# Performance work log

Hardware: AMD Instinct MI355X
Metric: run time of the kernel (lower is better)

## Reference

```python
import jax, jax.numpy as jnp
import numpy as np

B, NQ, NC, D, H = 4, 4096, 4096, 1024, 16
HD = D // H
LN_EPS = 1e-5


def _layernorm(x, g, b):
    mu = jnp.mean(x, axis=-1, keepdims=True)
    var = jnp.var(x, axis=-1, keepdims=True)
    return (x - mu) * jax.lax.rsqrt(var + LN_EPS) * g + b


def _kernel(x):
    # elu(x) + 1  (strictly positive feature map)
    return jax.nn.elu(x) + 1.0


def setup_inputs() -> dict:
    key = jax.random.key(0)
    ks = jax.random.split(key, 12)
    s = 1.0 / np.sqrt(D)
    return {
        "query": jax.random.normal(ks[0], (B, NQ, D), jnp.float32),
        "context": jax.random.normal(ks[1], (B, NC, D), jnp.float32),
        "q_w": jax.random.uniform(ks[2], (D, D), jnp.float32, -s, s),
        "q_b": jnp.zeros((D,), jnp.float32),
        "k_w": jax.random.uniform(ks[3], (D, D), jnp.float32, -s, s),
        "k_b": jnp.zeros((D,), jnp.float32),
        "v_w": jax.random.uniform(ks[4], (D, D), jnp.float32, -s, s),
        "v_b": jnp.zeros((D,), jnp.float32),
        "o_w": jax.random.uniform(ks[5], (D, D), jnp.float32, -s, s),
        "o_b": jnp.zeros((D,), jnp.float32),
        "lnq_g": jnp.ones((D,), jnp.float32),
        "lnq_b": jnp.zeros((D,), jnp.float32),
        "lnkv_g": jnp.ones((D,), jnp.float32),
        "lnkv_b": jnp.zeros((D,), jnp.float32),
    }


def reference(query, context, q_w, q_b, k_w, k_b, v_w, v_b, o_w, o_b,
              lnq_g, lnq_b, lnkv_g, lnkv_b):
    residual = query
    q = _layernorm(query, lnq_g, lnq_b)
    c = _layernorm(context, lnkv_g, lnkv_b)

    # torch Linear: y = x @ W.T + b ; reshape to (B, H, N, Hd)
    Q = (q @ q_w.T + q_b).reshape(B, NQ, H, HD).transpose(0, 2, 1, 3)
    K = (c @ k_w.T + k_b).reshape(B, NC, H, HD).transpose(0, 2, 1, 3)
    V = (c @ v_w.T + v_b).reshape(B, NC, H, HD).transpose(0, 2, 1, 3)

    Q = _kernel(Q)
    K = _kernel(K)

    # KV: (B, H, Hd, Hd) outer-product accumulation over context length
    KV = jnp.einsum("bhnd,bhne->bhde", K, V)
    K_sum = K.sum(axis=2)                              # (B, H, Hd)
    Z = jnp.einsum("bhqd,bhd->bhq", Q, K_sum)          # (B, H, Nq)
    Z = jnp.maximum(Z, 1e-6)

    out = jnp.einsum("bhqd,bhde->bhqe", Q, KV) / Z[..., None]
    out = out.transpose(0, 2, 1, 3).reshape(B, NQ, D)
    return residual + (out @ o_w.T + o_b)
```

## Files before the change

### kernel.cpp

```cpp
#include <hip/hip_runtime.h>

#define DEV __device__ __forceinline__

typedef __attribute__((ext_vector_type(8))) short short8;
typedef __attribute__((ext_vector_type(4))) short short4v;
typedef __attribute__((ext_vector_type(4))) float f32x4;

DEV float bf2f(unsigned short u) { return __uint_as_float(((unsigned int)u) << 16); }
DEV unsigned short f2bf(float f) {
    unsigned int u = __float_as_uint(f);
    u += 0x7FFFu + ((u >> 16) & 1u);
    return (unsigned short)(u >> 16);
}

DEV float elu1(float v) { return v > 0.0f ? v + 1.0f : __expf(v); }

DEV void gload_lds16(const void* g, void* l) {
    __builtin_amdgcn_global_load_lds(
        (__attribute__((address_space(1))) unsigned int*)(g),
        (__attribute__((address_space(3))) unsigned int*)(l),
        16, 0, 0);
}

#define NROW 16384
#define DDIM 1024

__global__ __launch_bounds__(256) void ln_kernel(
    const float* __restrict__ query, const float* __restrict__ context,
    const float* __restrict__ lnq_g, const float* __restrict__ lnq_b,
    const float* __restrict__ lnk_g, const float* __restrict__ lnk_b,
    unsigned short* __restrict__ qln, unsigned short* __restrict__ cln,
    const float* __restrict__ q_w, const float* __restrict__ k_w,
    const float* __restrict__ v_w, const float* __restrict__ o_w,
    unsigned short* __restrict__ wout)
{
    const int tid = threadIdx.x;
    if (blockIdx.x >= 2 * NROW) {
        const int i = (blockIdx.x - 2 * NROW) * 256 + tid;
        const int mat = i >> 18;
        const int idx = (i & 262143) * 4;
        const float* src = mat == 0 ? q_w : mat == 1 ? k_w : mat == 2 ? v_w : o_w;
        f32x4 v = *(const f32x4*)(src + idx);
        short4v o;
#pragma unroll
        for (int j = 0; j < 4; ++j) o[j] = (short)f2bf(v[j]);
        *(short4v*)(wout + (size_t)mat * 1048576 + idx) = o;
        return;
    }

    const int row = blockIdx.x;
    const bool isq = row < NROW;
    const int r = isq ? row : row - NROW;
    const float* src = (isq ? query : context) + (size_t)r * DDIM;
    const float* g   = isq ? lnq_g : lnk_g;
    const float* bb  = isq ? lnq_b : lnk_b;
    unsigned short* dst = (isq ? qln : cln) + (size_t)r * DDIM;

    f32x4 x = *(const f32x4*)(src + tid * 4);
    float s  = x[0] + x[1] + x[2] + x[3];
    float sq = x[0]*x[0] + x[1]*x[1] + x[2]*x[2] + x[3]*x[3];
#pragma unroll
    for (int off = 32; off; off >>= 1) {
        s  += __shfl_xor(s, off);
        sq += __shfl_xor(sq, off);
    }
    __shared__ float red[8];
    const int lane = tid & 63, w = tid >> 6;
    if (lane == 0) { red[w] = s; red[4 + w] = sq; }
    __syncthreads();
    s  = red[0] + red[1] + red[2] + red[3];
    sq = red[4] + red[5] + red[6] + red[7];
    const float mu  = s * (1.0f / DDIM);
    const float var = sq * (1.0f / DDIM) - mu * mu;
    const float rstd = rsqrtf(var + 1e-5f);

    f32x4 gv = *(const f32x4*)(g + tid * 4);
    f32x4 bv = *(const f32x4*)(bb + tid * 4);
    short4v o;
#pragma unroll
    for (int j = 0; j < 4; ++j)
        o[j] = (short)f2bf((x[j] - mu) * rstd * gv[j] + bv[j]);
    *(short4v*)(dst + tid * 4) = o;
}

template <typename EPI>
DEV void gemm128(unsigned short* __restrict__ sA,
                 unsigned short* __restrict__ sB,
                 const unsigned short* __restrict__ Ap,
                 const unsigned short* __restrict__ Bp,
                 int m0, int n0, EPI epi)
{
    const int tid = threadIdx.x;
    const int lane = tid & 63, w = tid >> 6;
    const int wr = w >> 1, wc = w & 1;
    const int lr = lane & 15, lg = lane >> 4;

    const int srow = tid >> 3;
    const int cswz = (tid & 7) ^ (srow & 7);
    const unsigned short* gA0 = Ap + (size_t)(m0 + srow) * 1024 + cswz * 8;
    const unsigned short* gB0 = Bp + (size_t)(n0 + srow) * 1024 + cswz * 8;
    unsigned short* dA = sA + tid * 8;
    unsigned short* dB = sB + tid * 8;

    const int sw0 = ((0 + lg) ^ (lr & 7)) * 8;
    const int sw1 = ((4 + lg) ^ (lr & 7)) * 8;

    f32x4 acc[4][4];
#pragma unroll
    for (int i = 0; i < 4; ++i)
#pragma unroll
        for (int j = 0; j < 4; ++j)
#pragma unroll
            for (int e = 0; e < 4; ++e) acc[i][j][e] = 0.0f;

#define STG8(T)                                                               \
    {                                                                         \
        const int ko = (T) * 64;                                              \
        _Pragma("unroll")                                                     \
        for (int j = 0; j < 4; ++j) {                                         \
            gload_lds16(gA0 + ko + (size_t)j * 32768, dA + j * 2048);         \
            gload_lds16(gB0 + ko + (size_t)j * 32768, dB + j * 2048);         \
        }                                                                     \
    }

    STG8(0);
    for (int t = 0; t < 16; ++t) {
        asm volatile("s_waitcnt vmcnt(0)" ::: "memory");
        __builtin_amdgcn_s_barrier();

        short8 af[4], bf[4];
#pragma unroll
        for (int mt = 0; mt < 4; ++mt)
            af[mt] = *(const short8*)&sA[(wr * 64 + mt * 16 + lr) * 64 + sw0];
#pragma unroll
        for (int nt = 0; nt < 4; ++nt)
            bf[nt] = *(const short8*)&sB[(wc * 64 + nt * 16 + lr) * 64 + sw0];
        __builtin_amdgcn_s_setprio(1);
#pragma unroll
        for (int mt = 0; mt < 4; ++mt)
#pragma unroll
            for (int nt = 0; nt < 4; ++nt)
                acc[mt][nt] = __builtin_amdgcn_mfma_f32_16x16x32_bf16(
                    af[mt], bf[nt], acc[mt][nt], 0, 0, 0);
        __builtin_amdgcn_s_setprio(0);

#pragma unroll
        for (int mt = 0; mt < 4; ++mt)
            af[mt] = *(const short8*)&sA[(wr * 64 + mt * 16 + lr) * 64 + sw1];
#pragma unroll
        for (int nt = 0; nt < 4; ++nt)
            bf[nt] = *(const short8*)&sB[(wc * 64 + nt * 16 + lr) * 64 + sw1];
        asm volatile("s_waitcnt lgkmcnt(0)" ::: "memory");
        __builtin_amdgcn_s_barrier();
        if (t < 15) STG8(t + 1);
        __builtin_amdgcn_s_setprio(1);
#pragma unroll
        for (int mt = 0; mt < 4; ++mt)
#pragma unroll
            for (int nt = 0; nt < 4; ++nt)
                acc[mt][nt] = __builtin_amdgcn_mfma_f32_16x16x32_bf16(
                    af[mt], bf[nt], acc[mt][nt], 0, 0, 0);
        __builtin_amdgcn_s_setprio(0);
    }
#undef STG8

#pragma unroll
    for (int mt = 0; mt < 4; ++mt)
#pragma unroll
        for (int nt = 0; nt < 4; ++nt) {
            const int col = n0 + wc * 64 + nt * 16 + lr;
#pragma unroll
            for (int i = 0; i < 4; ++i) {
                const int row = m0 + wr * 64 + mt * 16 + lg * 4 + i;
                epi(row, col, acc[mt][nt][i]);
            }
        }
}

__global__ __launch_bounds__(256, 4) void gemm_qkv(
    const unsigned short* __restrict__ QLN, const unsigned short* __restrict__ WQ,
    const unsigned short* __restrict__ CLN, const unsigned short* __restrict__ WKV,
    unsigned short* __restrict__ Qm, unsigned short* __restrict__ KVT,
    const float* __restrict__ q_b, const float* __restrict__ k_b,
    const float* __restrict__ v_b)
{
    __shared__ __attribute__((aligned(16))) unsigned short sA[128 * 64];
    __shared__ __attribute__((aligned(16))) unsigned short sB[128 * 64];

    const int bid = blockIdx.x;
    const int l = (bid & 7) * 384 + (bid >> 3);

    if (l < 1024) {
        const int m0 = (l >> 3) * 128, n0 = (l & 7) * 128;
        gemm128(sA, sB, QLN, WQ, m0, n0,
            [&](int row, int col, float v) {
                v = elu1(v + q_b[col]);
                Qm[(size_t)row * 1024 + col] = f2bf(v);
            });
    } else {
        const int r = l - 1024;
        const int m0 = (r & 15) * 128, n0 = (r >> 4) * 128;
        gemm128(sA, sB, WKV, CLN, m0, n0,
            [&](int row, int col, float v) {
                if (row < 1024) v = elu1(v + k_b[row]);
                else            v = v + v_b[row - 1024];
                KVT[(size_t)row * NROW + col] = f2bf(v);
            });
    }
}

__global__ __launch_bounds__(512, 2) void gemm_out256(
    const unsigned short* __restrict__ A, const unsigned short* __restrict__ Bm,
    float* __restrict__ Cout, const float* __restrict__ bias,
    const float* __restrict__ resid)
{
    __shared__ __attribute__((aligned(16))) unsigned short smem[65536];
    unsigned short* sAb = smem;
    unsigned short* sBb = smem + 32768;

    const int bid = blockIdx.x;
    const int l = (bid & 7) * 32 + (bid >> 3);
    const int m0 = (l >> 2) * 256, n0 = (l & 3) * 256;

    const int tid = threadIdx.x;
    const int lane = tid & 63, w = tid >> 6;
    const int wr = w >> 2, wc = w & 3;
    const int lr = lane & 15, lg = lane >> 4;

    const int srow = tid >> 3;
    const int cswz = (tid & 7) ^ (srow & 7);
    const unsigned short* gA0 = A  + (size_t)(m0 + srow) * 1024 + cswz * 8;
    const unsigned short* gB0 = Bm + (size_t)(n0 + srow) * 1024 + cswz * 8;

    const int sw0 = ((0 + lg) ^ (lr & 7)) * 8;
    const int sw1 = ((4 + lg) ^ (lr & 7)) * 8;

    f32x4 acc[8][4];
#pragma unroll
    for (int i = 0; i < 8; ++i)
#pragma unroll
        for (int j = 0; j < 4; ++j)
#pragma unroll
            for (int e = 0; e < 4; ++e) acc[i][j][e] = 0.0f;

#define STG(GP, SP, T)                                                        \
    {                                                                         \
        const unsigned short* g = (GP) + (T) * 64;                            \
        unsigned short* d = (SP) + ((T) & 1) * 16384 + tid * 8;               \
        _Pragma("unroll")                                                     \
        for (int L = 0; L < 4; ++L)                                           \
            gload_lds16(g + (size_t)L * 65536, d + L * 4096);                 \
    }

    STG(gB0, sBb, 0); STG(gA0, sAb, 0); STG(gB0, sBb, 1); STG(gA0, sAb, 1);
    asm volatile("s_waitcnt vmcnt(8)" ::: "memory");
    __builtin_amdgcn_s_barrier();

    short8 bvl[2][2];
#pragma unroll
    for (int nt = 0; nt < 2; ++nt) {
        const int rb = (wc * 64 + nt * 16 + lr) * 64;
        bvl[nt][0] = *(const short8*)&sBb[rb + sw0];
        bvl[nt][1] = *(const short8*)&sBb[rb + sw1];
    }

    for (int t = 0; t < 16; ++t) {
        const unsigned short* bA = sAb + (t & 1) * 16384;
        const unsigned short* bB = sBb + (t & 1) * 16384;
        const unsigned short* bBn = sBb + ((t + 1) & 1) * 16384;
        short8 afl[4][2], afh[4][2], bvh[2][2], bvln[2][2];

#pragma unroll
        for (int mt = 0; mt < 4; ++mt) {
            const int ra = (wr * 128 + mt * 16 + lr) * 64;
            afl[mt][0] = *(const short8*)&bA[ra + sw0];
            afl[mt][1] = *(const short8*)&bA[ra + sw1];
        }
#pragma unroll
        for (int mt = 0; mt < 4; ++mt) {
            const int ra = (wr * 128 + (mt + 4) * 16 + lr) * 64;
            afh[mt][0] = *(const short8*)&bA[ra + sw0];
            afh[mt][1] = *(const short8*)&bA[ra + sw1];
        }
        asm volatile("s_waitcnt lgkmcnt(8)" ::: "memory");
        __builtin_amdgcn_s_setprio(1);
#pragma unroll
        for (int kk = 0; kk < 2; ++kk)
#pragma unroll
            for (int mt = 0; mt < 4; ++mt)
#pragma unroll
                for (int nt = 0; nt < 2; ++nt)
                    acc[mt][nt] = __builtin_amdgcn_mfma_f32_16x16x32_bf16(
                        afl[mt][kk], bvl[nt][kk], acc[mt][nt], 0, 0, 0);
        __builtin_amdgcn_s_setprio(0);
        __builtin_amdgcn_s_barrier();

#pragma unroll
        for (int nt = 0; nt < 2; ++nt) {
            const int rb = (wc * 64 + (nt + 2) * 16 + lr) * 64;
            bvh[nt][0] = *(const short8*)&bB[rb + sw0];
            bvh[nt][1] = *(const short8*)&bB[rb + sw1];
        }
        asm volatile("s_waitcnt lgkmcnt(4)" ::: "memory");
        __builtin_amdgcn_s_setprio(1);
#pragma unroll
        for (int kk = 0; kk < 2; ++kk)
#pragma unroll
            for (int mt = 0; mt < 4; ++mt)
#pragma unroll
                for (int nt = 0; nt < 2; ++nt)
                    acc[mt + 4][nt] = __builtin_amdgcn_mfma_f32_16x16x32_bf16(
                        afh[mt][kk], bvl[nt][kk], acc[mt + 4][nt], 0, 0, 0);
        __builtin_amdgcn_s_setprio(0);
        asm volatile("s_waitcnt vmcnt(0)" ::: "memory");
        __builtin_amdgcn_s_barrier();

        if (t < 15) {
#pragma unroll
            for (int nt = 0; nt < 2; ++nt) {
                const int rb = (wc * 64 + nt * 16 + lr) * 64;
                bvln[nt][0] = *(const short8*)&bBn[rb + sw0];
                bvln[nt][1] = *(const short8*)&bBn[rb + sw1];
            }
        }
        if (t + 2 < 16) STG(gA0, sAb, t + 2);
        if (t < 15) asm volatile("s_waitcnt lgkmcnt(4)" ::: "memory");
        else        asm volatile("s_waitcnt lgkmcnt(0)" ::: "memory");
        __builtin_amdgcn_s_setprio(1);
#pragma unroll
        for (int kk = 0; kk < 2; ++kk)
#pragma unroll
            for (int mt = 0; mt < 4; ++mt)
#pragma unroll
                for (int nt = 0; nt < 2; ++nt)
                    acc[mt + 4][nt + 2] = __builtin_amdgcn_mfma_f32_16x16x32_bf16(
                        afh[mt][kk], bvh[nt][kk], acc[mt + 4][nt + 2], 0, 0, 0);
        __builtin_amdgcn_s_setprio(0);
        __builtin_amdgcn_s_barrier();

        if (t + 2 < 16) STG(gB0, sBb, t + 2);
        __builtin_amdgcn_s_setprio(1);
#pragma unroll
        for (int kk = 0; kk < 2; ++kk)
#pragma unroll
            for (int mt = 0; mt < 4; ++mt)
#pragma unroll
                for (int nt = 0; nt < 2; ++nt)
                    acc[mt][nt + 2] = __builtin_amdgcn_mfma_f32_16x16x32_bf16(
                        afl[mt][kk], bvh[nt][kk], acc[mt][nt + 2], 0, 0, 0);
        __builtin_amdgcn_s_setprio(0);

        if (t < 15) {
#pragma unroll
            for (int nt = 0; nt < 2; ++nt) {
                bvl[nt][0] = bvln[nt][0];
                bvl[nt][1] = bvln[nt][1];
            }
        }
    }
#undef STG

#pragma unroll
    for (int mt = 0; mt < 8; ++mt) {
#pragma unroll
        for (int nt = 0; nt < 4; ++nt) {
            const int col = n0 + wc * 64 + nt * 16 + lr;
#pragma unroll
            for (int i = 0; i < 4; ++i) {
                const int row = m0 + wr * 128 + mt * 16 + lg * 4 + i;
                Cout[(size_t)row * 1024 + col] =
                    acc[mt][nt][i] + bias[col] + resid[(size_t)row * 1024 + col];
            }
        }
    }
}

__global__ __launch_bounds__(256) void kv_kernel(
    const unsigned short* __restrict__ VT, const unsigned short* __restrict__ KT,
    float* __restrict__ KVTp, float* __restrict__ Ksump)
{
    const int bh = blockIdx.x, sp = blockIdx.y;
    const int b = bh >> 4, h = bh & 15;
    const int tid = threadIdx.x, lane = tid & 63, w = tid >> 6;
    const int lr = lane & 15, lg = lane >> 4;

    f32x4 acc[4][4];
#pragma unroll
    for (int i = 0; i < 4; ++i)
#pragma unroll
        for (int j = 0; j < 4; ++j)
#pragma unroll
            for (int e = 0; e < 4; ++e) acc[i][j][e] = 0.0f;
    float kp[4] = {0.0f, 0.0f, 0.0f, 0.0f};

    const size_t colbase = (size_t)b * 4096 + sp * 512 + w * 128 + lg * 8;
    const unsigned short* va = VT + (size_t)(h * 64 + lr) * NROW + colbase;
    const unsigned short* ka = KT + (size_t)(h * 64 + lr) * NROW + colbase;

    for (int ks = 0; ks < 4; ++ks) {
        short8 af[4], bfv[4];
#pragma unroll
        for (int mt = 0; mt < 4; ++mt)
            af[mt] = *(const short8*)(va + (size_t)mt * 16 * NROW + ks * 32);
#pragma unroll
        for (int nt = 0; nt < 4; ++nt)
            bfv[nt] = *(const short8*)(ka + (size_t)nt * 16 * NROW + ks * 32);
#pragma unroll
        for (int mt = 0; mt < 4; ++mt)
#pragma unroll
            for (int nt = 0; nt < 4; ++nt)
                acc[mt][nt] = __builtin_amdgcn_mfma_f32_16x16x32_bf16(
                    af[mt], bfv[nt], acc[mt][nt], 0, 0, 0);
#pragma unroll
        for (int nt = 0; nt < 4; ++nt)
#pragma unroll
            for (int j = 0; j < 8; ++j)
                kp[nt] += bf2f((unsigned short)bfv[nt][j]);
    }

#pragma unroll
    for (int nt = 0; nt < 4; ++nt) {
        kp[nt] += __shfl_xor(kp[nt], 16);
        kp[nt] += __shfl_xor(kp[nt], 32);
    }
    __shared__ float kred[4][64];
    if (lane < 16) {
#pragma unroll
        for (int nt = 0; nt < 4; ++nt) kred[w][nt * 16 + lane] = kp[nt];
    }

    __shared__ float red4[4][4096];
#pragma unroll
    for (int mt = 0; mt < 4; ++mt)
#pragma unroll
        for (int nt = 0; nt < 4; ++nt)
#pragma unroll
            for (int i = 0; i < 4; ++i)
                red4[w][(mt * 16 + lg * 4 + i) * 64 + nt * 16 + lr] = acc[mt][nt][i];
    __syncthreads();
    float* out = KVTp + ((size_t)sp * 64 + bh) * 4096;
    for (int i = tid; i < 4096; i += 256)
        out[i] = red4[0][i] + red4[1][i] + red4[2][i] + red4[3][i];
    if (tid < 64)
        Ksump[((size_t)sp * 64 + bh) * 64 + tid] =
            kred[0][tid] + kred[1][tid] + kred[2][tid] + kred[3][tid];
}

__global__ __launch_bounds__(256) void kvred_kernel(
    const float* __restrict__ KVTp, const float* __restrict__ Ksump,
    float* __restrict__ KVs, float* __restrict__ Ks)
{
    const int bh = blockIdx.x;
    const int tid = threadIdx.x;
    for (int i = tid * 4; i < 4096; i += 1024) {
        f32x4 s = {0.0f, 0.0f, 0.0f, 0.0f};
#pragma unroll
        for (int sp = 0; sp < 8; ++sp) {
            f32x4 v = *(const f32x4*)(KVTp + ((size_t)sp * 64 + bh) * 4096 + i);
            s[0] += v[0]; s[1] += v[1]; s[2] += v[2]; s[3] += v[3];
        }
        *(f32x4*)(KVs + (size_t)bh * 4096 + i) = s;
    }
    if (tid < 64) {
        float s = 0.0f;
#pragma unroll
        for (int sp = 0; sp < 8; ++sp)
            s += Ksump[((size_t)sp * 64 + bh) * 64 + tid];
        Ks[bh * 64 + tid] = s;
    }
}

__global__ __launch_bounds__(256) void a2_kernel(
    const unsigned short* __restrict__ Q, const float* __restrict__ KVs,
    const float* __restrict__ Ks, unsigned short* __restrict__ A2)
{
    const int m0 = blockIdx.x * 128, h = blockIdx.y;
    const int b = m0 >> 12, bh = (b << 4) + h;
    const int tid = threadIdx.x, lane = tid & 63, w = tid >> 6;
    const int wr = w >> 1, wc = w & 1;
    const int lr = lane & 15, lg = lane >> 4;

    __shared__ float ksum_s[64];
    if (tid < 64) ksum_s[tid] = Ks[bh * 64 + tid];
    __syncthreads();

    f32x4 acc[4][2];
#pragma unroll
    for (int i = 0; i < 4; ++i)
#pragma unroll
        for (int j = 0; j < 2; ++j)
#pragma unroll
            for (int e = 0; e < 4; ++e) acc[i][j][e] = 0.0f;
    float zp[4] = {0.0f, 0.0f, 0.0f, 0.0f};

    const unsigned short* qa = Q + (size_t)(m0 + wr * 64 + lr) * DDIM + h * 64 + lg * 8;
    const float* kvb = KVs + (size_t)bh * 4096 + (wc * 32 + lr) * 64 + lg * 8;

#pragma unroll
    for (int ks = 0; ks < 2; ++ks) {
        short8 af[4];
#pragma unroll
        for (int mt = 0; mt < 4; ++mt)
            af[mt] = *(const short8*)(qa + (size_t)mt * 16 * DDIM + ks * 32);
#pragma unroll
        for (int mt = 0; mt < 4; ++mt)
#pragma unroll
            for (int j = 0; j < 8; ++j)
                zp[mt] += bf2f((unsigned short)af[mt][j]) * ksum_s[ks * 32 + lg * 8 + j];
        short8 bfv[2];
#pragma unroll
        for (int nt = 0; nt < 2; ++nt) {
            const float* p = kvb + nt * 16 * 64 + ks * 32;
            f32x4 v0 = *(const f32x4*)(p);
            f32x4 v1 = *(const f32x4*)(p + 4);
            short8 t;
#pragma unroll
            for (int j = 0; j < 4; ++j) {
                t[j]     = (short)f2bf(v0[j]);
                t[j + 4] = (short)f2bf(v1[j]);
            }
            bfv[nt] = t;
        }
#pragma unroll
        for (int mt = 0; mt < 4; ++mt)
#pragma unroll
            for (int nt = 0; nt < 2; ++nt)
                acc[mt][nt] = __builtin_amdgcn_mfma_f32_16x16x32_bf16(
                    af[mt], bfv[nt], acc[mt][nt], 0, 0, 0);
    }

    float zinv[4];
#pragma unroll
    for (int mt = 0; mt < 4; ++mt) {
        zp[mt] += __shfl_xor(zp[mt], 16);
        zp[mt] += __shfl_xor(zp[mt], 32);
        zinv[mt] = 1.0f / fmaxf(zp[mt], 1e-6f);
    }

#pragma unroll
    for (int mt = 0; mt < 4; ++mt)
#pragma unroll
        for (int nt = 0; nt < 2; ++nt)
#pragma unroll
            for (int i = 0; i < 4; ++i) {
                const int row = m0 + wr * 64 + mt * 16 + lg * 4 + i;
                const int col = h * 64 + wc * 32 + nt * 16 + lr;
                const float zi = __shfl(zinv[mt], lg * 4 + i);
                const float v = acc[mt][nt][i] * zi;
                A2[(size_t)row * DDIM + col] = f2bf(v);
            }
}

extern "C" void kernel_launch(void* const* d_in, const int* in_sizes, int n_in,
                              void* d_out, int out_size, void* d_ws, size_t ws_size,
                              hipStream_t stream)
{
    const float* query   = (const float*)d_in[0];
    const float* context = (const float*)d_in[1];
    const float* q_w = (const float*)d_in[2];
    const float* q_b = (const float*)d_in[3];
    const float* k_w = (const float*)d_in[4];
    const float* k_b = (const float*)d_in[5];
    const float* v_w = (const float*)d_in[6];
    const float* v_b = (const float*)d_in[7];
    const float* o_w = (const float*)d_in[8];
    const float* o_b = (const float*)d_in[9];
    const float* lnq_g = (const float*)d_in[10];
    const float* lnq_b = (const float*)d_in[11];
    const float* lnk_g = (const float*)d_in[12];
    const float* lnk_b = (const float*)d_in[13];

    char* ws = (char*)d_ws;
    unsigned short* WQ  = (unsigned short*)(ws);
    unsigned short* WKV = (unsigned short*)(ws + (2u << 20));
    unsigned short* WO  = (unsigned short*)(ws + (6u << 20));
    unsigned short* QLN = (unsigned short*)(ws + (8u << 20));
    unsigned short* CLN = (unsigned short*)(ws + (40u << 20));
    unsigned short* Qm  = (unsigned short*)(ws + (72u << 20));
    unsigned short* KT  = (unsigned short*)(ws + (104u << 20));
    unsigned short* VT  = (unsigned short*)(ws + (136u << 20));
    float* KVTp  = (float*)(ws + (168u << 20));
    float* Ksump = (float*)(ws + (176u << 20));
    float* KVs   = (float*)(ws + (177u << 20));
    float* Ks    = (float*)(ws + (178u << 20));
    unsigned short* A2 = QLN;

    ln_kernel<<<2 * NROW + 4096, 256, 0, stream>>>(
        query, context, lnq_g, lnq_b, lnk_g, lnk_b, QLN, CLN,
        q_w, k_w, v_w, o_w, WQ);
    gemm_qkv<<<3072, 256, 0, stream>>>(QLN, WQ, CLN, WKV, Qm, KT,
                                       q_b, k_b, v_b);
    kv_kernel<<<dim3(64, 8), 256, 0, stream>>>(VT, KT, KVTp, Ksump);
    kvred_kernel<<<64, 256, 0, stream>>>(KVTp, Ksump, KVs, Ks);
    a2_kernel<<<dim3(128, 16), 256, 0, stream>>>(Qm, KVs, Ks, A2);
    gemm_out256<<<256, 512, 0, stream>>>(A2, WO, (float*)d_out, o_b, query);
}
```

Measured before the change: 277.9 us.

## Use one wavefront per LayerNorm row and split KV reduction by output quadrants

LayerNorm now gives each wavefront a whole row, which removes the shared-memory cross-wave reduction and the block barrier. The KV outer-product kernel now has each wave own a 32x32 quadrant of the 64x64 output instead of reducing partials over waves through a 64KB LDS buffer. It doubles the context splits to 16 so occupancy stays up, and kvred sums 16 partials instead of 8. The scratch buffers move into the CLN region, which is dead after gemm_qkv, so the workspace is smaller and stays hotter in cache. The cost is more partial-sum traffic.

```diff
diff --git a/kernel.cpp b/kernel.cpp
--- a/kernel.cpp
+++ b/kernel.cpp
@@ -35,8 +35,8 @@
     unsigned short* __restrict__ wout)
 {
     const int tid = threadIdx.x;
-    if (blockIdx.x >= 2 * NROW) {
-        const int i = (blockIdx.x - 2 * NROW) * 256 + tid;
+    if (blockIdx.x >= 8192) {
+        const int i = (blockIdx.x - 8192) * 256 + tid;
         const int mat = i >> 18;
         const int idx = (i & 262143) * 4;
         const float* src = mat == 0 ? q_w : mat == 1 ? k_w : mat == 2 ? v_w : o_w;
@@ -48,7 +48,8 @@
         return;
     }
 
-    const int row = blockIdx.x;
+    const int lane = tid & 63, w = tid >> 6;
+    const int row = blockIdx.x * 4 + w;
     const bool isq = row < NROW;
     const int r = isq ? row : row - NROW;
     const float* src = (isq ? query : context) + (size_t)r * DDIM;
@@ -56,31 +57,33 @@
     const float* bb  = isq ? lnq_b : lnk_b;
     unsigned short* dst = (isq ? qln : cln) + (size_t)r * DDIM;
 
-    f32x4 x = *(const f32x4*)(src + tid * 4);
-    float s  = x[0] + x[1] + x[2] + x[3];
-    float sq = x[0]*x[0] + x[1]*x[1] + x[2]*x[2] + x[3]*x[3];
+    f32x4 x[4];
+    float s = 0.0f, sq = 0.0f;
+#pragma unroll
+    for (int j = 0; j < 4; ++j) {
+        x[j] = *(const f32x4*)(src + j * 256 + lane * 4);
+#pragma unroll
+        for (int e = 0; e < 4; ++e) { s += x[j][e]; sq += x[j][e] * x[j][e]; }
+    }
 #pragma unroll
     for (int off = 32; off; off >>= 1) {
         s  += __shfl_xor(s, off);
         sq += __shfl_xor(sq, off);
     }
-    __shared__ float red[8];
-    const int lane = tid & 63, w = tid >> 6;
-    if (lane == 0) { red[w] = s; red[4 + w] = sq; }
-    __syncthreads();
-    s  = red[0] + red[1] + red[2] + red[3];
-    sq = red[4] + red[5] + red[6] + red[7];
     const float mu  = s * (1.0f / DDIM);
     const float var = sq * (1.0f / DDIM) - mu * mu;
     const float rstd = rsqrtf(var + 1e-5f);
 
-    f32x4 gv = *(const f32x4*)(g + tid * 4);
-    f32x4 bv = *(const f32x4*)(bb + tid * 4);
-    short4v o;
-#pragma unroll
-    for (int j = 0; j < 4; ++j)
-        o[j] = (short)f2bf((x[j] - mu) * rstd * gv[j] + bv[j]);
-    *(short4v*)(dst + tid * 4) = o;
+#pragma unroll
+    for (int j = 0; j < 4; ++j) {
+        f32x4 gv = *(const f32x4*)(g  + j * 256 + lane * 4);
+        f32x4 bv = *(const f32x4*)(bb + j * 256 + lane * 4);
+        short4v o;
+#pragma unroll
+        for (int e = 0; e < 4; ++e)
+            o[e] = (short)f2bf((x[j][e] - mu) * rstd * gv[e] + bv[e]);
+        *(short4v*)(dst + j * 256 + lane * 4) = o;
+    }
 }
 
 template <typename EPI>
@@ -383,67 +386,64 @@
     const int b = bh >> 4, h = bh & 15;
     const int tid = threadIdx.x, lane = tid & 63, w = tid >> 6;
     const int lr = lane & 15, lg = lane >> 4;
-
-    f32x4 acc[4][4];
-#pragma unroll
-    for (int i = 0; i < 4; ++i)
-#pragma unroll
-        for (int j = 0; j < 4; ++j)
+    const int eh = (w >> 1) * 32, dh = (w & 1) * 32;
+
+    f32x4 acc[2][2];
+#pragma unroll
+    for (int i = 0; i < 2; ++i)
+#pragma unroll
+        for (int j = 0; j < 2; ++j)
 #pragma unroll
             for (int e = 0; e < 4; ++e) acc[i][j][e] = 0.0f;
-    float kp[4] = {0.0f, 0.0f, 0.0f, 0.0f};
-
-    const size_t colbase = (size_t)b * 4096 + sp * 512 + w * 128 + lg * 8;
-    const unsigned short* va = VT + (size_t)(h * 64 + lr) * NROW + colbase;
-    const unsigned short* ka = KT + (size_t)(h * 64 + lr) * NROW + colbase;
-
-    for (int ks = 0; ks < 4; ++ks) {
-        short8 af[4], bfv[4];
-#pragma unroll
-        for (int mt = 0; mt < 4; ++mt)
-            af[mt] = *(const short8*)(va + (size_t)mt * 16 * NROW + ks * 32);
-#pragma unroll
-        for (int nt = 0; nt < 4; ++nt)
-            bfv[nt] = *(const short8*)(ka + (size_t)nt * 16 * NROW + ks * 32);
-#pragma unroll
-        for (int mt = 0; mt < 4; ++mt)
-#pragma unroll
-            for (int nt = 0; nt < 4; ++nt)
+    float kp[2] = {0.0f, 0.0f};
+
+    const size_t colbase = (size_t)b * 4096 + sp * 256 + lg * 8;
+    const unsigned short* va = VT + (size_t)(h * 64 + eh + lr) * NROW + colbase;
+    const unsigned short* ka = KT + (size_t)(h * 64 + dh + lr) * NROW + colbase;
+
+    for (int ks = 0; ks < 8; ++ks) {
+        short8 af[2], bfv[2];
+        af[0]  = *(const short8*)(va + ks * 32);
+        af[1]  = *(const short8*)(va + (size_t)16 * NROW + ks * 32);
+        bfv[0] = *(const short8*)(ka + ks * 32);
+        bfv[1] = *(const short8*)(ka + (size_t)16 * NROW + ks * 32);
+#pragma unroll
+        for (int mt = 0; mt < 2; ++mt)
+#pragma unroll
+            for (int nt = 0; nt < 2; ++nt)
                 acc[mt][nt] = __builtin_amdgcn_mfma_f32_16x16x32_bf16(
                     af[mt], bfv[nt], acc[mt][nt], 0, 0, 0);
-#pragma unroll
-        for (int nt = 0; nt < 4; ++nt)
-#pragma unroll
-            for (int j = 0; j < 8; ++j)
-                kp[nt] += bf2f((unsigned short)bfv[nt][j]);
-    }
-
-#pragma unroll
-    for (int nt = 0; nt < 4; ++nt) {
-        kp[nt] += __shfl_xor(kp[nt], 16);
-        kp[nt] += __shfl_xor(kp[nt], 32);
-    }
-    __shared__ float kred[4][64];
-    if (lane < 16) {
-#pragma unroll
-        for (int nt = 0; nt < 4; ++nt) kred[w][nt * 16 + lane] = kp[nt];
-    }
-
-    __shared__ float red4[4][4096];
-#pragma unroll
-    for (int mt = 0; mt < 4; ++mt)
-#pragma unroll
-        for (int nt = 0; nt < 4; ++nt)
+        if (w < 2) {
+#pragma unroll
+            for (int nt = 0; nt < 2; ++nt)
+#pragma unroll
+                for (int j = 0; j < 8; ++j)
+                    kp[nt] += bf2f((unsigned short)bfv[nt][j]);
+        }
+    }
+
+    float* out = KVTp + ((size_t)sp * 64 + bh) * 4096;
+#pragma unroll
+    for (int mt = 0; mt < 2; ++mt)
+#pragma unroll
+        for (int nt = 0; nt < 2; ++nt)
 #pragma unroll
             for (int i = 0; i < 4; ++i)
-                red4[w][(mt * 16 + lg * 4 + i) * 64 + nt * 16 + lr] = acc[mt][nt][i];
-    __syncthreads();
-    float* out = KVTp + ((size_t)sp * 64 + bh) * 4096;
-    for (int i = tid; i < 4096; i += 256)
-        out[i] = red4[0][i] + red4[1][i] + red4[2][i] + red4[3][i];
-    if (tid < 64)
-        Ksump[((size_t)sp * 64 + bh) * 64 + tid] =
-            kred[0][tid] + kred[1][tid] + kred[2][tid] + kred[3][tid];
+                out[(eh + mt * 16 + lg * 4 + i) * 64 + dh + nt * 16 + lr] =
+                    acc[mt][nt][i];
+
+    if (w < 2) {
+#pragma unroll
+        for (int nt = 0; nt < 2; ++nt) {
+            kp[nt] += __shfl_xor(kp[nt], 16);
+            kp[nt] += __shfl_xor(kp[nt], 32);
+        }
+        if (lane < 16) {
+#pragma unroll
+            for (int nt = 0; nt < 2; ++nt)
+                Ksump[((size_t)sp * 64 + bh) * 64 + dh + nt * 16 + lane] = kp[nt];
+        }
+    }
 }
 
 __global__ __launch_bounds__(256) void kvred_kernel(
@@ -455,7 +455,7 @@
     for (int i = tid * 4; i < 4096; i += 1024) {
         f32x4 s = {0.0f, 0.0f, 0.0f, 0.0f};
 #pragma unroll
-        for (int sp = 0; sp < 8; ++sp) {
+        for (int sp = 0; sp < 16; ++sp) {
             f32x4 v = *(const f32x4*)(KVTp + ((size_t)sp * 64 + bh) * 4096 + i);
             s[0] += v[0]; s[1] += v[1]; s[2] += v[2]; s[3] += v[3];
         }
@@ -464,7 +464,7 @@
     if (tid < 64) {
         float s = 0.0f;
 #pragma unroll
-        for (int sp = 0; sp < 8; ++sp)
+        for (int sp = 0; sp < 16; ++sp)
             s += Ksump[((size_t)sp * 64 + bh) * 64 + tid];
         Ks[bh * 64 + tid] = s;
     }
@@ -579,18 +579,18 @@
     unsigned short* Qm  = (unsigned short*)(ws + (72u << 20));
     unsigned short* KT  = (unsigned short*)(ws + (104u << 20));
     unsigned short* VT  = (unsigned short*)(ws + (136u << 20));
-    float* KVTp  = (float*)(ws + (168u << 20));
-    float* Ksump = (float*)(ws + (176u << 20));
-    float* KVs   = (float*)(ws + (177u << 20));
-    float* Ks    = (float*)(ws + (178u << 20));
+    float* KVTp  = (float*)(ws + (40u << 20));
+    float* Ksump = (float*)(ws + (56u << 20));
+    float* KVs   = (float*)(ws + (57u << 20));
+    float* Ks    = (float*)(ws + (58u << 20));
     unsigned short* A2 = QLN;
 
-    ln_kernel<<<2 * NROW + 4096, 256, 0, stream>>>(
+    ln_kernel<<<8192 + 4096, 256, 0, stream>>>(
         query, context, lnq_g, lnq_b, lnk_g, lnk_b, QLN, CLN,
         q_w, k_w, v_w, o_w, WQ);
     gemm_qkv<<<3072, 256, 0, stream>>>(QLN, WQ, CLN, WKV, Qm, KT,
                                        q_b, k_b, v_b);
-    kv_kernel<<<dim3(64, 8), 256, 0, stream>>>(VT, KT, KVTp, Ksump);
+    kv_kernel<<<dim3(64, 16), 256, 0, stream>>>(VT, KT, KVTp, Ksump);
     kvred_kernel<<<64, 256, 0, stream>>>(KVTp, Ksump, KVs, Ks);
     a2_kernel<<<dim3(128, 16), 256, 0, stream>>>(Qm, KVs, Ks, A2);
     gemm_out256<<<256, 512, 0, stream>>>(A2, WO, (float*)d_out, o_b, query);
```

Result: faster. 265.9 us (median of 3 runs) (-4.3%).
